# Optimization experiments

Measured on AMD Instinct MI355X. Metric: run time of the kernel, lower is better.

Reference implementation:

```python
import jax, jax.numpy as jnp
import numpy as np

EMBED_DIM = 1024
NUM_HEADS = 16
HEAD_DIM = EMBED_DIM // NUM_HEADS
SCALE = 1.0 / np.sqrt(HEAD_DIM)


def _quant_linear(x, w, b):
    # Per-tensor symmetric int8 quantize -> dequantize -> GEMM (faithful to QuantizedLinear)
    s = jnp.max(jnp.abs(w)) / 127.0
    w_dq = jnp.clip(jnp.round(w / s), -128.0, 127.0) * s
    return jnp.einsum('bse,oe->bso', x, w_dq) + b


def setup_inputs() -> dict:
    key = jax.random.key(0)
    ks = jax.random.split(key, 7)
    B, S, E = 2, 2048, EMBED_DIM
    return {
        'query': jax.random.normal(ks[0], (B, S, E), dtype=jnp.float32),
        'key': jax.random.normal(ks[1], (B, S, E), dtype=jnp.float32),
        'value': jax.random.normal(ks[2], (B, S, E), dtype=jnp.float32),
        'Wq': jax.random.normal(ks[3], (E, E), dtype=jnp.float32) * 0.02,
        'bq': jnp.zeros((E,), dtype=jnp.float32),
        'Wk': jax.random.normal(ks[4], (E, E), dtype=jnp.float32) * 0.02,
        'bk': jnp.zeros((E,), dtype=jnp.float32),
        'Wv': jax.random.normal(ks[5], (E, E), dtype=jnp.float32) * 0.02,
        'bv': jnp.zeros((E,), dtype=jnp.float32),
        'Wo': jax.random.normal(ks[6], (E, E), dtype=jnp.float32) * 0.02,
        'bo': jnp.zeros((E,), dtype=jnp.float32),
    }


def reference(query, key, value, Wq, bq, Wk, bk, Wv, bv, Wo, bo):
    B, S, E = query.shape
    H, D = NUM_HEADS, HEAD_DIM
    Q = _quant_linear(query, Wq, bq).reshape(B, S, H, D).transpose(0, 2, 1, 3)
    K = _quant_linear(key, Wk, bk).reshape(B, S, H, D).transpose(0, 2, 1, 3)
    V = _quant_linear(value, Wv, bv).reshape(B, S, H, D).transpose(0, 2, 1, 3)
    # [B,H,S,S] unfused attention scores
    scores = jnp.einsum('bhqd,bhkd->bhqk', Q, K) * SCALE
    attn = jax.nn.softmax(scores, axis=-1)  # dropout is identity at inference
    out = jnp.einsum('bhqk,bhkd->bhqd', attn, V)
    out = out.transpose(0, 2, 1, 3).reshape(B, S, E)
    return _quant_linear(out, Wo, bo)
```

## Files before the change

kernel.cpp:

```cpp
#include <hip/hip_runtime.h>
#include <math.h>

#define S_LEN 2048
#define EMB   1024
#define NHEAD 16
#define HDIM  64
#define MTOT  4096
#define EXP2_SCALE 0.18033688011112042f

typedef __attribute__((ext_vector_type(8))) short bf16x8;
typedef __attribute__((ext_vector_type(4))) float f32x4;

#if __has_builtin(__builtin_amdgcn_exp2f)
#define FEXP2(x) __builtin_amdgcn_exp2f(x)
#else
#define FEXP2(x) exp2f(x)
#endif

__device__ __forceinline__ short f2bf(float f) {
  union { float f; unsigned u; } v; v.f = f;
  unsigned r = v.u + 0x7fffu + ((v.u >> 16) & 1u);
  return (short)(r >> 16);
}
__device__ __forceinline__ float bf2f(short s) {
  union { float f; unsigned u; } v; v.u = ((unsigned)(unsigned short)s) << 16;
  return v.f;
}
__device__ __forceinline__ unsigned pkbf(float e0, float e1) {
  unsigned a = __float_as_uint(e1) + 0x8000u;
  unsigned b = __float_as_uint(e0) + 0x8000u;
  return __builtin_amdgcn_perm(a, b, 0x07060302u);
}

__device__ __forceinline__ void gload_lds16(const void* g, void* l) {
  __builtin_amdgcn_global_load_lds(
      (const __attribute__((address_space(1))) void*)g,
      (__attribute__((address_space(3))) void*)l, 16, 0, 0);
}

__global__ void wabsmax_k(const float* __restrict__ W0, const float* __restrict__ W1,
                          const float* __restrict__ W2, const float* __restrict__ W3,
                          unsigned* __restrict__ scaleU) {
  int w = blockIdx.x & 3;
  int part = blockIdx.x >> 2;
  const float* W = (w == 0) ? W0 : (w == 1) ? W1 : (w == 2) ? W2 : W3;
  float m = 0.f;
  int base = part * 16384;
#pragma unroll
  for (int p = 0; p < 16; ++p) {
    const float4 v = *(const float4*)&W[base + p * 1024 + threadIdx.x * 4];
    m = fmaxf(m, fmaxf(fmaxf(fabsf(v.x), fabsf(v.y)), fmaxf(fabsf(v.z), fabsf(v.w))));
  }
  __shared__ float red[256];
  red[threadIdx.x] = m;
  __syncthreads();
  for (int s = 128; s > 0; s >>= 1) {
    if (threadIdx.x < s) red[threadIdx.x] = fmaxf(red[threadIdx.x], red[threadIdx.x + s]);
    __syncthreads();
  }
  if (threadIdx.x == 0) atomicMax(&scaleU[w], __float_as_uint(red[0]));
}

__global__ void wquant_k(const float* __restrict__ W0, const float* __restrict__ W1,
                         const float* __restrict__ W2, const float* __restrict__ W3,
                         short* __restrict__ Q0, short* __restrict__ Q1,
                         short* __restrict__ Q2, short* __restrict__ Q3,
                         const unsigned* __restrict__ scaleU, float* __restrict__ sVal) {
  int w = blockIdx.y;
  const float* W = (w == 0) ? W0 : (w == 1) ? W1 : (w == 2) ? W2 : W3;
  short* Q = (w == 0) ? Q0 : (w == 1) ? Q1 : (w == 2) ? Q2 : Q3;
  float s = __uint_as_float(scaleU[w]) * (1.0f / 127.0f);
  if (blockIdx.x == 0 && threadIdx.x == 0) sVal[w] = s;
  int idx = (blockIdx.x * 256 + threadIdx.x) * 4;
  float4 v = *(const float4*)&W[idx];
  short4 q;
  q.x = f2bf(fminf(fmaxf(rintf(v.x / s), -128.f), 127.f));
  q.y = f2bf(fminf(fmaxf(rintf(v.y / s), -128.f), 127.f));
  q.z = f2bf(fminf(fmaxf(rintf(v.z / s), -128.f), 127.f));
  q.w = f2bf(fminf(fmaxf(rintf(v.w / s), -128.f), 127.f));
  *(short4*)&Q[idx] = q;
}

__global__ void acast_k(const float* __restrict__ A0, const float* __restrict__ A1,
                        const float* __restrict__ A2,
                        short* __restrict__ H0, short* __restrict__ H1,
                        short* __restrict__ H2) {
  int w = blockIdx.y;
  const float* A = (w == 0) ? A0 : (w == 1) ? A1 : A2;
  short* H = (w == 0) ? H0 : (w == 1) ? H1 : H2;
  int idx = (blockIdx.x * 256 + threadIdx.x) * 4;
  float4 v = *(const float4*)&A[idx];
  short4 h;
  h.x = f2bf(v.x); h.y = f2bf(v.y); h.z = f2bf(v.z); h.w = f2bf(v.w);
  *(short4*)&H[idx] = h;
}

__device__ __forceinline__ void gemm_core(
    const short* __restrict__ Ah, const short* __restrict__ Bq, int m0, int n0,
    short* AhS, short* BsS, f32x4 acc[4][4]) {
  const int tid = threadIdx.x;
  const int lane = tid & 63, wave = tid >> 6;
  const int quad = lane >> 4, l16 = lane & 15;
  const int wm = wave >> 1, wn = wave & 1;

  const int swrow = lane >> 2, swcol = (lane & 3) * 8;
  const short* agh = Ah + (m0 + wave * 32 + swrow) * 1024 + swcol;
  const short* bgp = Bq + (n0 + wave * 32 + swrow) * 1024 + swcol;
  short* sA0 = AhS + wave * 1024;
  short* sB0 = BsS + wave * 1024;

  for (int k0 = 0; k0 < 1024; k0 += 32) {
    __syncthreads();
    gload_lds16(agh + k0,             sA0);
    gload_lds16(agh + 16 * 1024 + k0, sA0 + 512);
    gload_lds16(bgp + k0,             sB0);
    gload_lds16(bgp + 16 * 1024 + k0, sB0 + 512);
    __syncthreads();
    bf16x8 ah[4], bb[4];
#pragma unroll
    for (int mi = 0; mi < 4; ++mi) {
      int row = wm * 64 + mi * 16 + l16;
      ah[mi] = *(const bf16x8*)&AhS[row * 32 + quad * 8];
    }
#pragma unroll
    for (int ni = 0; ni < 4; ++ni) {
      int row = wn * 64 + ni * 16 + l16;
      bb[ni] = *(const bf16x8*)&BsS[row * 32 + quad * 8];
    }
#pragma unroll
    for (int mi = 0; mi < 4; ++mi)
#pragma unroll
      for (int ni = 0; ni < 4; ++ni)
        acc[mi][ni] = __builtin_amdgcn_mfma_f32_16x16x32_bf16(ah[mi], bb[ni], acc[mi][ni], 0, 0, 0);
  }
}

__global__ __launch_bounds__(256, 2) void gemm_qkv(
    const short* __restrict__ QA, const short* __restrict__ KA, const short* __restrict__ VA,
    const short* __restrict__ WqQ, const short* __restrict__ WkQ, const short* __restrict__ WvQ,
    const float* __restrict__ sVal,
    const float* __restrict__ bq, const float* __restrict__ bk, const float* __restrict__ bv,
    short* __restrict__ Qh, short* __restrict__ Kh, short* __restrict__ Vh) {
  __shared__ __align__(16) short AhS[128 * 32];
  __shared__ __align__(16) short BsS[128 * 32];
  const int z = blockIdx.z;
  const short* Ah = (z == 0) ? QA : (z == 1) ? KA : VA;
  const short* Bq = (z == 0) ? WqQ : (z == 1) ? WkQ : WvQ;
  const float* bias = (z == 0) ? bq : (z == 1) ? bk : bv;
  short* oh = (z == 0) ? Qh : (z == 1) ? Kh : Vh;

  const int m0 = blockIdx.y * 128, n0 = blockIdx.x * 128;
  f32x4 acc[4][4];
#pragma unroll
  for (int i = 0; i < 4; ++i)
#pragma unroll
    for (int j = 0; j < 4; ++j) acc[i][j] = (f32x4){0.f, 0.f, 0.f, 0.f};

  gemm_core(Ah, Bq, m0, n0, AhS, BsS, acc);

  const int lane = threadIdx.x & 63, wave = threadIdx.x >> 6;
  const int quad = lane >> 4, l16 = lane & 15;
  const int wm = wave >> 1, wn = wave & 1;
  float s = sVal[z];
  float post = (z == 0) ? EXP2_SCALE : 1.0f;
#pragma unroll
  for (int mi = 0; mi < 4; ++mi) {
#pragma unroll
    for (int ni = 0; ni < 4; ++ni) {
      int rowb = m0 + wm * 64 + mi * 16 + quad * 4;
      int col = n0 + wn * 64 + ni * 16 + l16;
      float bia = bias[col];
      int h = col >> 6, d = col & 63;
      if (z < 2) {
#pragma unroll
        for (int r = 0; r < 4; ++r) {
          float v = (acc[mi][ni][r] * s + bia) * post;
          int row = rowb + r;
          int b = row >> 11, sq = row & 2047;
          oh[((b * 16 + h) * 2048 + sq) * 64 + d] = f2bf(v);
        }
      } else {
        int b = rowb >> 11, sq = rowb & 2047;
        short4 pk;
        pk.x = f2bf(acc[mi][ni][0] * s + bia);
        pk.y = f2bf(acc[mi][ni][1] * s + bia);
        pk.z = f2bf(acc[mi][ni][2] * s + bia);
        pk.w = f2bf(acc[mi][ni][3] * s + bia);
        *(short4*)&oh[((b * 16 + h) * 64 + d) * 2048 + sq] = pk;
      }
    }
  }
}

__global__ __launch_bounds__(256, 2) void gemm_o(
    const short* __restrict__ OAh, const short* __restrict__ OAl,
    const short* __restrict__ WoQ, const float* __restrict__ sPtr,
    const float* __restrict__ bias, float* __restrict__ outF) {
  __shared__ __align__(16) short AhS[128 * 32];
  __shared__ __align__(16) short AlS[128 * 32];
  __shared__ __align__(16) short BsS[64 * 32];
  const int tid = threadIdx.x;
  const int lane = tid & 63, wave = tid >> 6;
  const int quad = lane >> 4, l16 = lane & 15;
  const int m0 = blockIdx.y * 128, n0 = blockIdx.x * 64;

  f32x4 acc[2][4];
#pragma unroll
  for (int i = 0; i < 2; ++i)
#pragma unroll
    for (int j = 0; j < 4; ++j) acc[i][j] = (f32x4){0.f, 0.f, 0.f, 0.f};

  const int swrow = lane >> 2, swcol = (lane & 3) * 8;
  const short* agh = OAh + (m0 + wave * 32 + swrow) * 1024 + swcol;
  const short* agl = OAl + (m0 + wave * 32 + swrow) * 1024 + swcol;
  const short* bgp = WoQ + (n0 + wave * 16 + swrow) * 1024 + swcol;
  short* sA0 = AhS + wave * 1024;
  short* sA1 = AlS + wave * 1024;
  short* sB0 = BsS + wave * 512;

  for (int k0 = 0; k0 < 1024; k0 += 32) {
    __syncthreads();
    gload_lds16(agh + k0,             sA0);
    gload_lds16(agh + 16 * 1024 + k0, sA0 + 512);
    gload_lds16(agl + k0,             sA1);
    gload_lds16(agl + 16 * 1024 + k0, sA1 + 512);
    gload_lds16(bgp + k0,             sB0);
    __syncthreads();
    bf16x8 ah[2], al[2], bb[4];
#pragma unroll
    for (int mi = 0; mi < 2; ++mi) {
      int row = wave * 32 + mi * 16 + l16;
      ah[mi] = *(const bf16x8*)&AhS[row * 32 + quad * 8];
      al[mi] = *(const bf16x8*)&AlS[row * 32 + quad * 8];
    }
#pragma unroll
    for (int ni = 0; ni < 4; ++ni) {
      int row = ni * 16 + l16;
      bb[ni] = *(const bf16x8*)&BsS[row * 32 + quad * 8];
    }
#pragma unroll
    for (int mi = 0; mi < 2; ++mi)
#pragma unroll
      for (int ni = 0; ni < 4; ++ni) {
        acc[mi][ni] = __builtin_amdgcn_mfma_f32_16x16x32_bf16(ah[mi], bb[ni], acc[mi][ni], 0, 0, 0);
        acc[mi][ni] = __builtin_amdgcn_mfma_f32_16x16x32_bf16(al[mi], bb[ni], acc[mi][ni], 0, 0, 0);
      }
  }

  const float s = *sPtr;
#pragma unroll
  for (int mi = 0; mi < 2; ++mi) {
#pragma unroll
    for (int ni = 0; ni < 4; ++ni) {
      int rowb = m0 + wave * 32 + mi * 16 + quad * 4;
      int col = n0 + ni * 16 + l16;
      float bia = bias[col];
#pragma unroll
      for (int r = 0; r < 4; ++r)
        outF[(rowb + r) * 1024 + col] = acc[mi][ni][r] * s + bia;
    }
  }
}

__global__ __launch_bounds__(256, 2) void flash_k(
    const short* __restrict__ Qh, const short* __restrict__ Kh,
    const short* __restrict__ Vh,
    short* __restrict__ Ohi, short* __restrict__ Olo) {
  __shared__ __align__(16) short Khs[64 * 64];
  __shared__ __align__(16) short Vhs[64 * 64];

  const int tid = threadIdx.x;
  const int lane = tid & 63, wave = tid >> 6;
  const int quad = lane >> 4, l16 = lane & 15;
  const int bh = blockIdx.y;
  const int b = bh >> 4, h = bh & 15;
  const int q0 = blockIdx.x * 128 + wave * 32;
  const int qkbase = bh * (S_LEN * HDIM);
  const int vbase  = bh * (HDIM * S_LEN);

  bf16x8 qb[2][2];
#pragma unroll
  for (int g = 0; g < 2; ++g) {
    const int qrow = qkbase + (q0 + g * 16 + l16) * HDIM;
    qb[g][0] = *(const bf16x8*)&Qh[qrow + quad * 8];
    qb[g][1] = *(const bf16x8*)&Qh[qrow + 32 + quad * 8];
  }

  f32x4 zero = {0.f, 0.f, 0.f, 0.f};
  f32x4 oacc[2][4];
#pragma unroll
  for (int g = 0; g < 2; ++g)
#pragma unroll
    for (int i = 0; i < 4; ++i) oacc[g][i] = zero;
  f32x4 sacc[2] = {zero, zero};

  union { bf16x8 v; unsigned u[4]; } ones_;
  ones_.u[0] = ones_.u[1] = ones_.u[2] = ones_.u[3] = 0x3F803F80u;

  const int sr = tid >> 2, sc8 = (tid & 3) * 8;
  const int srP = (sr & 32) | (((sr >> 2) & 1) << 4) | (((sr >> 3) & 3) << 2) | (sr & 3);
  const int kgl = qkbase + sr * HDIM + sc8;
  const int vgl = vbase + sr * S_LEN + sc8;

  bf16x8 pk0 = *(const bf16x8*)&Kh[kgl];
  bf16x8 pk1 = *(const bf16x8*)&Kh[kgl + 32];
  bf16x8 pv0 = *(const bf16x8*)&Vh[vgl];
  bf16x8 pv1 = *(const bf16x8*)&Vh[vgl + 32];

#define SIDX(row, col) ((row) * 64 + ((col) ^ (((row) & 1) << 5)))

  for (int kt = 0; kt < S_LEN; kt += 64) {
    __syncthreads();
    *(bf16x8*)&Khs[SIDX(srP, sc8)]      = pk0;
    *(bf16x8*)&Khs[SIDX(srP, sc8 + 32)] = pk1;
    *(bf16x8*)&Vhs[SIDX(sr, sc8)]       = pv0;
    *(bf16x8*)&Vhs[SIDX(sr, sc8 + 32)]  = pv1;
    __syncthreads();
    if (kt + 64 < S_LEN) {
      int kg = kgl + (kt + 64) * HDIM;
      int vg = vgl + (kt + 64);
      pk0 = *(const bf16x8*)&Kh[kg];
      pk1 = *(const bf16x8*)&Kh[kg + 32];
      pv0 = *(const bf16x8*)&Vh[vg];
      pv1 = *(const bf16x8*)&Vh[vg + 32];
    }
    f32x4 sc[2][4];
#pragma unroll
    for (int nj = 0; nj < 4; ++nj) {
      const int kr = nj * 16 + l16;
      bf16x8 kf0 = *(const bf16x8*)&Khs[SIDX(kr, quad * 8)];
      bf16x8 kf1 = *(const bf16x8*)&Khs[SIDX(kr, 32 + quad * 8)];
#pragma unroll
      for (int g = 0; g < 2; ++g) {
        f32x4 sv = zero;
        sv = __builtin_amdgcn_mfma_f32_16x16x32_bf16(kf0, qb[g][0], sv, 0, 0, 0);
        sv = __builtin_amdgcn_mfma_f32_16x16x32_bf16(kf1, qb[g][1], sv, 0, 0, 0);
        sc[g][nj] = sv;
      }
    }
#pragma unroll
    for (int g = 0; g < 2; ++g)
#pragma unroll
      for (int nj = 0; nj < 4; ++nj)
#pragma unroll
        for (int r = 0; r < 4; ++r)
          sc[g][nj][r] = FEXP2(sc[g][nj][r]);
    union { bf16x8 v; unsigned u[4]; } P[2][2];
#pragma unroll
    for (int g = 0; g < 2; ++g) {
      P[g][0].u[0] = pkbf(sc[g][0][0], sc[g][0][1]);
      P[g][0].u[1] = pkbf(sc[g][0][2], sc[g][0][3]);
      P[g][0].u[2] = pkbf(sc[g][1][0], sc[g][1][1]);
      P[g][0].u[3] = pkbf(sc[g][1][2], sc[g][1][3]);
      P[g][1].u[0] = pkbf(sc[g][2][0], sc[g][2][1]);
      P[g][1].u[1] = pkbf(sc[g][2][2], sc[g][2][3]);
      P[g][1].u[2] = pkbf(sc[g][3][0], sc[g][3][1]);
      P[g][1].u[3] = pkbf(sc[g][3][2], sc[g][3][3]);
    }
#pragma unroll
    for (int g = 0; g < 2; ++g) {
      sacc[g] = __builtin_amdgcn_mfma_f32_16x16x32_bf16(P[g][0].v, ones_.v, sacc[g], 0, 0, 0);
      sacc[g] = __builtin_amdgcn_mfma_f32_16x16x32_bf16(P[g][1].v, ones_.v, sacc[g], 0, 0, 0);
    }
#pragma unroll
    for (int ni = 0; ni < 4; ++ni) {
      int vr = ni * 16 + l16;
      bf16x8 vf0 = *(const bf16x8*)&Vhs[SIDX(vr, quad * 8)];
      bf16x8 vf1 = *(const bf16x8*)&Vhs[SIDX(vr, 32 + quad * 8)];
#pragma unroll
      for (int g = 0; g < 2; ++g) {
        oacc[g][ni] = __builtin_amdgcn_mfma_f32_16x16x32_bf16(P[g][0].v, vf0, oacc[g][ni], 0, 0, 0);
        oacc[g][ni] = __builtin_amdgcn_mfma_f32_16x16x32_bf16(P[g][1].v, vf1, oacc[g][ni], 0, 0, 0);
      }
    }
  }
#undef SIDX
#pragma unroll
  for (int g = 0; g < 2; ++g) {
#pragma unroll
    for (int r = 0; r < 4; ++r) {
      float inv = 1.f / sacc[g][r];
      int row = b * S_LEN + q0 + g * 16 + quad * 4 + r;
#pragma unroll
      for (int ni = 0; ni < 4; ++ni) {
        float v = oacc[g][ni][r] * inv;
        int idx = row * 1024 + h * 64 + ni * 16 + l16;
        short hi = f2bf(v);
        Ohi[idx] = hi;
        Olo[idx] = f2bf(v - bf2f(hi));
      }
    }
  }
}

extern "C" void kernel_launch(void* const* d_in, const int* in_sizes, int n_in,
                              void* d_out, int out_size, void* d_ws, size_t ws_size,
                              hipStream_t stream) {
  const float* query = (const float*)d_in[0];
  const float* key_i = (const float*)d_in[1];
  const float* value = (const float*)d_in[2];
  const float* Wq = (const float*)d_in[3];
  const float* bq = (const float*)d_in[4];
  const float* Wk = (const float*)d_in[5];
  const float* bk = (const float*)d_in[6];
  const float* Wv = (const float*)d_in[7];
  const float* bv = (const float*)d_in[8];
  const float* Wo = (const float*)d_in[9];
  const float* bo = (const float*)d_in[10];
  float* out = (float*)d_out;

  char* w = (char*)d_ws;
  unsigned* scaleU = (unsigned*)w;
  float* sVal = (float*)(w + 256);
  size_t off = 512;
  const size_t SZ_W = 2097152;
  const size_t SZ_A = 8388608;
  short* WqQ = (short*)(w + off); off += SZ_W;
  short* WkQ = (short*)(w + off); off += SZ_W;
  short* WvQ = (short*)(w + off); off += SZ_W;
  short* WoQ = (short*)(w + off); off += SZ_W;
  short* Qa  = (short*)(w + off); off += SZ_A;
  short* Ka  = (short*)(w + off); off += SZ_A;
  short* Va  = (short*)(w + off); off += SZ_A;
  short* Qh  = (short*)(w + off); off += SZ_A;
  short* Kh  = (short*)(w + off); off += SZ_A;
  short* Vh  = (short*)(w + off); off += SZ_A;
  short* Ohi = Qa;
  short* Olo = Ka;

  (void)hipMemsetAsync(scaleU, 0, 16, stream);
  wabsmax_k<<<256, 256, 0, stream>>>(Wq, Wk, Wv, Wo, scaleU);
  wquant_k<<<dim3(1024, 4), 256, 0, stream>>>(Wq, Wk, Wv, Wo, WqQ, WkQ, WvQ, WoQ, scaleU, sVal);
  acast_k<<<dim3(4096, 3), 256, 0, stream>>>(query, key_i, value, Qa, Ka, Va);
  gemm_qkv<<<dim3(8, 32, 3), 256, 0, stream>>>(Qa, Ka, Va, WqQ, WkQ, WvQ, sVal,
                                               bq, bk, bv, Qh, Kh, Vh);
  flash_k<<<dim3(16, 32), 256, 0, stream>>>(Qh, Kh, Vh, Ohi, Olo);
  gemm_o<<<dim3(16, 32), 256, 0, stream>>>(Ohi, Olo, WoQ, sVal + 3, bo, out);
}
```

Baseline: 244.0 us.

## Double-buffer K/V shared tiles with padded stride in flash attention kernel

Shared-memory K and V tiles become double-buffered, so each iteration ends with one barrier instead of two. The next tile is written into the alternate buffer after compute. The XOR swizzle is replaced by a padded row stride of 72, and the global-load thread mapping is changed to wave/lane-based rows. This doubles LDS use per block, which may limit occupancy, and the padding changes the LDS bank-conflict pattern.

New measurement: 255.9 us. 1.05x slower.

```diff
diff --git a/kernel.cpp b/kernel.cpp
--- a/kernel.cpp
+++ b/kernel.cpp
@@ -266,8 +266,8 @@
     const short* __restrict__ Qh, const short* __restrict__ Kh,
     const short* __restrict__ Vh,
     short* __restrict__ Ohi, short* __restrict__ Olo) {
-  __shared__ __align__(16) short Khs[64 * 64];
-  __shared__ __align__(16) short Vhs[64 * 64];
+  __shared__ __align__(16) short Khs[2][64 * 72];
+  __shared__ __align__(16) short Vhs[2][64 * 72];
 
   const int tid = threadIdx.x;
   const int lane = tid & 63, wave = tid >> 6;
@@ -297,39 +297,44 @@
   union { bf16x8 v; unsigned u[4]; } ones_;
   ones_.u[0] = ones_.u[1] = ones_.u[2] = ones_.u[3] = 0x3F803F80u;
 
-  const int sr = tid >> 2, sc8 = (tid & 3) * 8;
+  const int sr  = wave * 16 + l16;
+  const int sc8 = quad * 8;
   const int srP = (sr & 32) | (((sr >> 2) & 1) << 4) | (((sr >> 3) & 3) << 2) | (sr & 3);
   const int kgl = qkbase + sr * HDIM + sc8;
   const int vgl = vbase + sr * S_LEN + sc8;
+  const int kOff = srP * 72 + sc8;
+  const int vOff = sr * 72 + sc8;
 
   bf16x8 pk0 = *(const bf16x8*)&Kh[kgl];
   bf16x8 pk1 = *(const bf16x8*)&Kh[kgl + 32];
   bf16x8 pv0 = *(const bf16x8*)&Vh[vgl];
   bf16x8 pv1 = *(const bf16x8*)&Vh[vgl + 32];
 
-#define SIDX(row, col) ((row) * 64 + ((col) ^ (((row) & 1) << 5)))
-
+  *(bf16x8*)&Khs[0][kOff]      = pk0;
+  *(bf16x8*)&Khs[0][kOff + 32] = pk1;
+  *(bf16x8*)&Vhs[0][vOff]      = pv0;
+  *(bf16x8*)&Vhs[0][vOff + 32] = pv1;
+  __syncthreads();
+
+  int cur = 0;
   for (int kt = 0; kt < S_LEN; kt += 64) {
-    __syncthreads();
-    *(bf16x8*)&Khs[SIDX(srP, sc8)]      = pk0;
-    *(bf16x8*)&Khs[SIDX(srP, sc8 + 32)] = pk1;
-    *(bf16x8*)&Vhs[SIDX(sr, sc8)]       = pv0;
-    *(bf16x8*)&Vhs[SIDX(sr, sc8 + 32)]  = pv1;
-    __syncthreads();
-    if (kt + 64 < S_LEN) {
-      int kg = kgl + (kt + 64) * HDIM;
-      int vg = vgl + (kt + 64);
+    const bool more = (kt + 64 < S_LEN);
+    if (more) {
+      const int kg = kgl + (kt + 64) * HDIM;
+      const int vg = vgl + (kt + 64);
       pk0 = *(const bf16x8*)&Kh[kg];
       pk1 = *(const bf16x8*)&Kh[kg + 32];
       pv0 = *(const bf16x8*)&Vh[vg];
       pv1 = *(const bf16x8*)&Vh[vg + 32];
     }
+    const short* Kc = Khs[cur];
+    const short* Vc = Vhs[cur];
     f32x4 sc[2][4];
 #pragma unroll
     for (int nj = 0; nj < 4; ++nj) {
       const int kr = nj * 16 + l16;
-      bf16x8 kf0 = *(const bf16x8*)&Khs[SIDX(kr, quad * 8)];
-      bf16x8 kf1 = *(const bf16x8*)&Khs[SIDX(kr, 32 + quad * 8)];
+      bf16x8 kf0 = *(const bf16x8*)&Kc[kr * 72 + quad * 8];
+      bf16x8 kf1 = *(const bf16x8*)&Kc[kr * 72 + 32 + quad * 8];
 #pragma unroll
       for (int g = 0; g < 2; ++g) {
         f32x4 sv = zero;
@@ -365,16 +370,25 @@
 #pragma unroll
     for (int ni = 0; ni < 4; ++ni) {
       int vr = ni * 16 + l16;
-      bf16x8 vf0 = *(const bf16x8*)&Vhs[SIDX(vr, quad * 8)];
-      bf16x8 vf1 = *(const bf16x8*)&Vhs[SIDX(vr, 32 + quad * 8)];
+      bf16x8 vf0 = *(const bf16x8*)&Vc[vr * 72 + quad * 8];
+      bf16x8 vf1 = *(const bf16x8*)&Vc[vr * 72 + 32 + quad * 8];
 #pragma unroll
       for (int g = 0; g < 2; ++g) {
         oacc[g][ni] = __builtin_amdgcn_mfma_f32_16x16x32_bf16(P[g][0].v, vf0, oacc[g][ni], 0, 0, 0);
         oacc[g][ni] = __builtin_amdgcn_mfma_f32_16x16x32_bf16(P[g][1].v, vf1, oacc[g][ni], 0, 0, 0);
       }
     }
-  }
-#undef SIDX
+    if (more) {
+      short* Kn = (short*)Khs[cur ^ 1];
+      short* Vn = (short*)Vhs[cur ^ 1];
+      *(bf16x8*)&Kn[kOff]      = pk0;
+      *(bf16x8*)&Kn[kOff + 32] = pk1;
+      *(bf16x8*)&Vn[vOff]      = pv0;
+      *(bf16x8*)&Vn[vOff + 32] = pv1;
+      __syncthreads();
+      cur ^= 1;
+    }
+  }
 #pragma unroll
   for (int g = 0; g < 2; ++g) {
 #pragma unroll
```
